# Kernel optimization log

Hardware: AMD Instinct MI355X
Metric: run time of the kernel (lower is better)

Reference implementation:

```python
import jax, jax.numpy as jnp
import numpy as np

H, D, BS = 32, 128, 64          # num_heads, head_dim, gate block_size
GATE_DIM = 64
GATE_TEMP = 2.0                 # _GATE_TARGET_TEMPERATURE
CLAMP_MIN, CLAMP_MAX = -50.0, 50.0


def _rotate_half(x):
    x1, x2 = jnp.split(x, 2, axis=-1)
    return jnp.concatenate([-x2, x1], axis=-1)


def setup_inputs() -> dict:
    key = jax.random.key(0)
    ks = jax.random.split(key, 8)
    B, S, E = 1, 2048, 4096
    hidden_states = jax.random.normal(ks[0], (B, S, E), jnp.float32) * 0.02
    # standard RoPE tables, [B, S, D]
    inv_freq = 1.0 / (10000.0 ** (jnp.arange(0, D, 2, dtype=jnp.float32) / D))
    freqs = jnp.arange(S, dtype=jnp.float32)[:, None] * inv_freq[None, :]
    emb = jnp.concatenate([freqs, freqs], axis=-1)
    cos = jnp.broadcast_to(jnp.cos(emb)[None], (B, S, D)).astype(jnp.float32)
    sin = jnp.broadcast_to(jnp.sin(emb)[None], (B, S, D)).astype(jnp.float32)
    Wq = jax.random.normal(ks[1], (E, E), jnp.float32) * 0.02
    Wk = jax.random.normal(ks[2], (E, E), jnp.float32) * 0.02
    Wv = jax.random.normal(ks[3], (E, E), jnp.float32) * 0.02
    Wo = jax.random.normal(ks[4], (E, E), jnp.float32) * 0.02
    Wg_q = jax.random.normal(ks[5], (GATE_DIM, D), jnp.float32) * 0.05
    Wg_k = jax.random.normal(ks[6], (GATE_DIM, D), jnp.float32) * 0.05
    return {"hidden_states": hidden_states, "cos": cos, "sin": sin,
            "Wq": Wq, "Wk": Wk, "Wv": Wv, "Wo": Wo,
            "Wg_q": Wg_q, "Wg_k": Wg_k}


def reference(hidden_states, cos, sin, Wq, Wk, Wv, Wo, Wg_q, Wg_k):
    B, S, E = hidden_states.shape
    scale = np.float32(1.0 / np.sqrt(D))

    # ---- base attention (training path: full dense attention w/ scores) ----
    q = (hidden_states @ Wq.T).reshape(B, S, H, D).transpose(0, 2, 1, 3)  # [B,H,S,D]
    k = (hidden_states @ Wk.T).reshape(B, S, H, D).transpose(0, 2, 1, 3)
    v = (hidden_states @ Wv.T).reshape(B, S, H, D).transpose(0, 2, 1, 3)

    # _apply_rotary_pos_emb: cos/sin are 3D [B,S,D] -> unsqueeze head dim
    c, s = cos[:, None], sin[:, None]
    q = q * c + _rotate_half(q) * s
    k = k * c + _rotate_half(k) * s

    scores = jnp.einsum('bhqd,bhkd->bhqk', q, k) * scale  # [B,H,S,S]
    causal = jnp.tril(jnp.ones((S, S), dtype=bool))
    scores = jnp.where(causal, scores, -jnp.inf)
    attn = jax.nn.softmax(scores, axis=-1)
    ctx = jnp.einsum('bhqk,bhkd->bhqd', attn, v)
    attn_output = ctx.transpose(0, 2, 1, 3).reshape(B, S, E) @ Wo.T

    # ---- _compute_gate_target: blockwise maxpool -> clamp -> tempered softmax ----
    NB = S // BS  # S divisible by BS, so the -inf padding branch is a no-op
    block_max = scores.reshape(B, H, NB, BS, NB, BS).max(axis=(3, 5))  # [B,H,NB,NB]
    finite = jnp.isfinite(block_max)
    block_max = jnp.where(finite, jnp.clip(block_max, CLAMP_MIN, CLAMP_MAX), block_max)
    gate_target = jax.nn.softmax(
        block_max.reshape(B, H, NB * NB) / GATE_TEMP, axis=-1
    ).reshape(B, H, NB, NB)

    # ---- AttnGate prediction: mean-pooled block Q/K -> low-rank block logits ----
    qb = q.reshape(B, H, NB, BS, D).mean(axis=3)  # [B,H,NB,D]
    kb = k.reshape(B, H, NB, BS, D).mean(axis=3)
    gq = jnp.einsum('bhnd,gd->bhng', qb, Wg_q)
    gk = jnp.einsum('bhnd,gd->bhng', kb, Wg_k)
    glogits = jnp.einsum('bhqg,bhkg->bhqk', gq, gk) * np.float32(1.0 / np.sqrt(GATE_DIM))
    bmask = jnp.tril(jnp.ones((NB, NB), dtype=bool))  # block-causal
    glogits = jnp.where(bmask, glogits, -jnp.inf)
    gate_pred = jax.nn.softmax(
        glogits.reshape(B, H, NB * NB), axis=-1
    ).reshape(B, H, NB, NB)

    return attn_output, gate_pred, gate_target
```

## Files before the change

### kernel.cpp

```cpp
#include <hip/hip_runtime.h>
#include <stdint.h>

#define S_LEN 2048
#define EMB   4096
#define NHEAD 32
#define DHEAD 128
#define NBLK  32
#define GDIM  64

typedef float  f32x4  __attribute__((ext_vector_type(4)));
typedef __bf16 bf16x8 __attribute__((ext_vector_type(8)));
typedef unsigned short u16;

__device__ __forceinline__ u16 f2bf(float f) {
  uint32_t u = __float_as_uint(f);
  u += 0x7fffu + ((u >> 16) & 1u);
  return (u16)(u >> 16);
}
__device__ __forceinline__ float bf2f(u16 u) {
  return __uint_as_float(((uint32_t)u) << 16);
}

__device__ __forceinline__ void ld_lds16(const u16* g, u16* l) {
  __builtin_amdgcn_global_load_lds((const __attribute__((address_space(1))) void*)g,
                                   (__attribute__((address_space(3))) void*)l, 16, 0, 0);
}

__global__ void conv_f32_bf16(const float* __restrict__ in, u16* __restrict__ out, int n4) {
  int i = blockIdx.x * 256 + threadIdx.x;
  if (i >= n4) return;
  float4 v = ((const float4*)in)[i];
  ushort4 o;
  o.x = f2bf(v.x); o.y = f2bf(v.y); o.z = f2bf(v.z); o.w = f2bf(v.w);
  ((ushort4*)out)[i] = o;
}

__global__ void conv3_f32_bf16(const float* __restrict__ a, const float* __restrict__ b,
                               const float* __restrict__ c, u16* __restrict__ oa,
                               u16* __restrict__ ob, u16* __restrict__ oc, int n4) {
  int i = blockIdx.x * 256 + threadIdx.x;
  if (i >= n4) return;
  const float* in = (blockIdx.y == 0) ? a : (blockIdx.y == 1) ? b : c;
  u16* out = (blockIdx.y == 0) ? oa : (blockIdx.y == 1) ? ob : oc;
  float4 v = ((const float4*)in)[i];
  ushort4 o;
  o.x = f2bf(v.x); o.y = f2bf(v.y); o.z = f2bf(v.z); o.w = f2bf(v.w);
  ((ushort4*)out)[i] = o;
}

__global__ void __launch_bounds__(512, 2) qkv_gemm_256(
    const u16* __restrict__ A, const u16* __restrict__ Bq, const u16* __restrict__ Bk,
    const u16* __restrict__ Bv, u16* __restrict__ outq, u16* __restrict__ outk,
    u16* __restrict__ outvt, const float* __restrict__ cosp, const float* __restrict__ sinp)
{
  extern __shared__ u16 lds[];

  const int tid  = threadIdx.x;
  const int w    = tid >> 6;
  const int lane = tid & 63;
  const int r    = lane & 15;
  const int qd   = lane >> 4;
  const int wr   = w >> 2;
  const int wc   = w & 3;
  const int hh   = wc >> 1;

  const int which = blockIdx.x >> 4;
  const int nt    = blockIdx.x & 15;
  const int m0    = blockIdx.y * 256;
  const int n0    = nt * 256;
  const int K     = EMB;
  const u16* Bm = (which == 0) ? Bq : (which == 1) ? Bk : Bv;

  const int swz0 = (qd ^ (r & 7)) * 8;
  const int swz1 = ((4 + qd) ^ (r & 7)) * 8;
  const int rowbaseA = (wr * 64 + r) * 64;
  const int rowbaseB = (hh * 64 + (wc & 1) * 16 + r) * 64;

  const int srw = tid >> 3;
  const int sgs = ((tid & 7) ^ (srw & 7)) * 8;
  const u16* pA0 = A + (size_t)(m0 + srw) * K + sgs;
  const int fm = ((srw >> 5) & 1) * 64 + (srw & 31);
  const u16* pB0 = Bm + (size_t)(n0 + fm) * K + sgs;

  f32x4 acc[8][4];
#pragma unroll
  for (int mi = 0; mi < 8; ++mi)
#pragma unroll
    for (int ni = 0; ni < 4; ++ni) acc[mi][ni] = (f32x4){0.f, 0.f, 0.f, 0.f};

  auto stA = [&](int tt, int half) {
    u16* d = lds + ((tt & 1) * 2 + half) * 8192 + w * 512;
    const u16* g = pA0 + (size_t)(half * 128) * K + tt * 64;
    ld_lds16(g, d);
    ld_lds16(g + (size_t)64 * K, d + 4096);
  };
  auto stB = [&](int tt, int half) {
    u16* d = lds + 32768 + ((tt & 1) * 2 + half) * 8192 + w * 512;
    const u16* g = pB0 + (size_t)(half * 32) * K + tt * 64;
    ld_lds16(g, d);
    ld_lds16(g + (size_t)128 * K, d + 4096);
  };

  stA(0, 0); stB(0, 0); stB(0, 1); stA(0, 1);
  asm volatile("s_waitcnt vmcnt(0)" ::: "memory");
  __builtin_amdgcn_s_barrier();

  for (int t = 0; t < 64; ++t) {
    const u16* bufA = lds + (t & 1) * 16384;
    const u16* bufB = lds + 32768 + (t & 1) * 16384;
    bf16x8 aF[4][2], bLo[2][2], bHi[2][2];

    {
      const u16* ab = bufA + rowbaseA;
      const u16* bb = bufB + rowbaseB;
#pragma unroll
      for (int mi = 0; mi < 4; ++mi) {
        aF[mi][0] = *(const bf16x8*)(ab + mi * 1024 + swz0);
        aF[mi][1] = *(const bf16x8*)(ab + mi * 1024 + swz1);
      }
#pragma unroll
      for (int ni = 0; ni < 2; ++ni) {
        bLo[ni][0] = *(const bf16x8*)(bb + ni * 2048 + swz0);
        bLo[ni][1] = *(const bf16x8*)(bb + ni * 2048 + swz1);
      }
    }
    if (t < 63) stA(t + 1, 0);
    __builtin_amdgcn_s_barrier();
    asm volatile("s_waitcnt lgkmcnt(0)" ::: "memory");
    __builtin_amdgcn_sched_barrier(0);
    __builtin_amdgcn_s_setprio(1);
#pragma unroll
    for (int mi = 0; mi < 4; ++mi)
#pragma unroll
      for (int ni = 0; ni < 2; ++ni) {
        acc[mi][ni] = __builtin_amdgcn_mfma_f32_16x16x32_bf16(aF[mi][0], bLo[ni][0], acc[mi][ni], 0, 0, 0);
        acc[mi][ni] = __builtin_amdgcn_mfma_f32_16x16x32_bf16(aF[mi][1], bLo[ni][1], acc[mi][ni], 0, 0, 0);
      }
    __builtin_amdgcn_s_setprio(0);
    if (t < 63) asm volatile("s_waitcnt vmcnt(4)" ::: "memory");
    else        asm volatile("s_waitcnt vmcnt(2)" ::: "memory");
    __builtin_amdgcn_s_barrier();

    {
      const u16* bb = bufB + 8192 + rowbaseB;
#pragma unroll
      for (int ni = 0; ni < 2; ++ni) {
        bHi[ni][0] = *(const bf16x8*)(bb + ni * 2048 + swz0);
        bHi[ni][1] = *(const bf16x8*)(bb + ni * 2048 + swz1);
      }
    }
    if (t < 63) stB(t + 1, 0);
    __builtin_amdgcn_s_barrier();
    asm volatile("s_waitcnt lgkmcnt(0)" ::: "memory");
    __builtin_amdgcn_sched_barrier(0);
    __builtin_amdgcn_s_setprio(1);
#pragma unroll
    for (int mi = 0; mi < 4; ++mi)
#pragma unroll
      for (int ni = 0; ni < 2; ++ni) {
        acc[mi][ni + 2] = __builtin_amdgcn_mfma_f32_16x16x32_bf16(aF[mi][0], bHi[ni][0], acc[mi][ni + 2], 0, 0, 0);
        acc[mi][ni + 2] = __builtin_amdgcn_mfma_f32_16x16x32_bf16(aF[mi][1], bHi[ni][1], acc[mi][ni + 2], 0, 0, 0);
      }
    __builtin_amdgcn_s_setprio(0);
    if (t < 63) asm volatile("s_waitcnt vmcnt(4)" ::: "memory");
    else        asm volatile("s_waitcnt vmcnt(0)" ::: "memory");
    __builtin_amdgcn_s_barrier();

    {
      const u16* ab = bufA + 8192 + rowbaseA;
#pragma unroll
      for (int mi = 0; mi < 4; ++mi) {
        aF[mi][0] = *(const bf16x8*)(ab + mi * 1024 + swz0);
        aF[mi][1] = *(const bf16x8*)(ab + mi * 1024 + swz1);
      }
    }
    if (t < 63) stB(t + 1, 1);
    __builtin_amdgcn_s_barrier();
    asm volatile("s_waitcnt lgkmcnt(0)" ::: "memory");
    __builtin_amdgcn_sched_barrier(0);
    __builtin_amdgcn_s_setprio(1);
#pragma unroll
    for (int mi = 0; mi < 4; ++mi)
#pragma unroll
      for (int ni = 0; ni < 2; ++ni) {
        acc[mi + 4][ni + 2] = __builtin_amdgcn_mfma_f32_16x16x32_bf16(aF[mi][0], bHi[ni][0], acc[mi + 4][ni + 2], 0, 0, 0);
        acc[mi + 4][ni + 2] = __builtin_amdgcn_mfma_f32_16x16x32_bf16(aF[mi][1], bHi[ni][1], acc[mi + 4][ni + 2], 0, 0, 0);
      }
    __builtin_amdgcn_s_setprio(0);
    __builtin_amdgcn_s_barrier();

    if (t < 63) stA(t + 1, 1);
    __builtin_amdgcn_s_barrier();
    __builtin_amdgcn_s_setprio(1);
#pragma unroll
    for (int mi = 0; mi < 4; ++mi)
#pragma unroll
      for (int ni = 0; ni < 2; ++ni) {
        acc[mi + 4][ni] = __builtin_amdgcn_mfma_f32_16x16x32_bf16(aF[mi][0], bLo[ni][0], acc[mi + 4][ni], 0, 0, 0);
        acc[mi + 4][ni] = __builtin_amdgcn_mfma_f32_16x16x32_bf16(aF[mi][1], bLo[ni][1], acc[mi + 4][ni], 0, 0, 0);
      }
    __builtin_amdgcn_s_setprio(0);
    if (t < 63) asm volatile("s_waitcnt vmcnt(4)" ::: "memory");
    __builtin_amdgcn_s_barrier();
  }

  if (which < 2) {
    u16* out = which ? outk : outq;
    const int hh_out = 2 * nt + hh;
#pragma unroll
    for (int mi = 0; mi < 8; ++mi) {
      const int rbase = m0 + (mi >> 2) * 128 + wr * 64 + (mi & 3) * 16 + qd * 4;
#pragma unroll
      for (int pp = 0; pp < 2; ++pp) {
        const int dlo = pp * 32 + (wc & 1) * 16 + r;
#pragma unroll
        for (int rg = 0; rg < 4; ++rg) {
          int srow = rbase + rg;
          float c = cosp[srow * DHEAD + dlo];
          float s = sinp[srow * DHEAD + dlo];
          float lo = acc[mi][pp * 2 + 0][rg], hi = acc[mi][pp * 2 + 1][rg];
          size_t base = ((size_t)hh_out * S_LEN + srow) * DHEAD;
          out[base + dlo]      = f2bf(lo * c - hi * s);
          out[base + dlo + 64] = f2bf(hi * c + lo * s);
        }
      }
    }
  } else {
    u16* lT = lds;
#pragma unroll
    for (int ch = 0; ch < 2; ++ch) {
      __syncthreads();
#pragma unroll
      for (int mq = 0; mq < 4; ++mq) {
        const int mi = ch * 4 + mq;
        const int lr = wr * 64 + mq * 16 + qd * 4;
#pragma unroll
        for (int ni = 0; ni < 4; ++ni) {
          const int col = hh * 128 + (ni >> 1) * 32 + (wc & 1) * 16 + (ni & 1) * 64 + r;
#pragma unroll
          for (int rg = 0; rg < 4; ++rg)
            lT[col * 136 + lr + rg] = f2bf(acc[mi][ni][rg]);
        }
      }
      __syncthreads();
      const int c = tid >> 1, sh = (tid & 1) * 64;
      const int hh2 = 2 * nt + (c >> 7), d = c & 127;
      size_t obase = ((size_t)hh2 * DHEAD + d) * S_LEN + m0 + ch * 128 + sh;
#pragma unroll
      for (int i8 = 0; i8 < 8; ++i8) {
        uint4 v = *(const uint4*)&lT[c * 136 + sh + i8 * 8];
        *(uint4*)&outvt[obase + i8 * 8] = v;
      }
    }
  }
}

__global__ void __launch_bounds__(256, 2) gemm_out(
    const u16* __restrict__ A, const u16* __restrict__ B, float* __restrict__ out)
{
  __shared__ u16 lA[128 * 32];
  __shared__ u16 lB[128 * 32];
  const int tid = threadIdx.x;
  const int w = tid >> 6, lane = tid & 63;
  const int r = lane & 15, qd = lane >> 4;
  const int m0 = blockIdx.y * 128, n0 = blockIdx.x * 128;
  const int K = EMB;

  f32x4 acc[2][8];
#pragma unroll
  for (int mi = 0; mi < 2; ++mi)
#pragma unroll
    for (int ni = 0; ni < 8; ++ni) acc[mi][ni] = (f32x4){0.f, 0.f, 0.f, 0.f};

  const u16* Ab = A + (size_t)(m0 + w * 16 + (lane >> 2)) * K + (lane & 3) * 8;
  const u16* Bb = B + (size_t)(n0 + w * 16 + (lane >> 2)) * K + (lane & 3) * 8;
  u16* lAb = &lA[(w * 16) * 32];
  u16* lBb = &lB[(w * 16) * 32];

  for (int k0 = 0; k0 < K; k0 += 32) {
    __syncthreads();
    ld_lds16(Ab + k0, lAb);
    ld_lds16(Ab + (size_t)64 * K + k0, lAb + 64 * 32);
    ld_lds16(Bb + k0, lBb);
    ld_lds16(Bb + (size_t)64 * K + k0, lBb + 64 * 32);
    __syncthreads();
    bf16x8 af0 = *(const bf16x8*)&lA[(w * 32 + r) * 32 + qd * 8];
    bf16x8 af1 = *(const bf16x8*)&lA[(w * 32 + 16 + r) * 32 + qd * 8];
#pragma unroll
    for (int ni = 0; ni < 8; ++ni) {
      bf16x8 bf = *(const bf16x8*)&lB[(ni * 16 + r) * 32 + qd * 8];
      acc[0][ni] = __builtin_amdgcn_mfma_f32_16x16x32_bf16(af0, bf, acc[0][ni], 0, 0, 0);
      acc[1][ni] = __builtin_amdgcn_mfma_f32_16x16x32_bf16(af1, bf, acc[1][ni], 0, 0, 0);
    }
  }
#pragma unroll
  for (int mi = 0; mi < 2; ++mi)
#pragma unroll
    for (int ni = 0; ni < 8; ++ni)
#pragma unroll
      for (int rg = 0; rg < 4; ++rg) {
        int srow = m0 + w * 32 + mi * 16 + qd * 4 + rg;
        out[(size_t)srow * EMB + n0 + ni * 16 + r] = acc[mi][ni][rg];
      }
}

__global__ void __launch_bounds__(256, 2) attn_fwd(
    const u16* __restrict__ qg, const u16* __restrict__ kg, const u16* __restrict__ vtg,
    u16* __restrict__ ctx, float* __restrict__ bmax)
{
  __shared__ u16 lK[2][64 * 128];
  __shared__ u16 lV[2][128 * 64];
  __shared__ u16 lP[64 * 76];
  __shared__ float lBM[4 * NBLK];

  const int tid = threadIdx.x;
  const int w = tid >> 6, lane = tid & 63;
  const int r = lane & 15, qd = lane >> 4;
  const int h = blockIdx.y;
  const u16* ksrc = kg + (size_t)h * S_LEN * DHEAD;
  const u16* vsrc = vtg + (size_t)h * DHEAD * S_LEN;
  const float scale = 0.08838834764831845f;

  const int ksl   = (lane & 15) ^ (w * 4 + (lane >> 4));
  const int krow0 = w * 4 + (lane >> 4);
  const u16* kg0  = ksrc + (size_t)krow0 * DHEAD + ksl * 8;
  const int vsl   = (lane & 7) ^ (lane >> 3);
  const int vrow0 = w * 8 + (lane >> 3);
  const u16* vg0  = vsrc + (size_t)vrow0 * S_LEN + vsl * 8;

  for (int qsel = 0; qsel < 2; ++qsel) {
    const int qb = qsel ? (31 - (int)blockIdx.x) : (int)blockIdx.x;

    auto stage = [&](int kb, int buf) {
      u16* kd = &lK[buf][w * 512];
      const u16* kgp = kg0 + (size_t)kb * 64 * DHEAD;
#pragma unroll
      for (int i = 0; i < 4; ++i) ld_lds16(kgp + i * 16 * DHEAD, kd + i * 2048);
      u16* vd = &lV[buf][w * 512];
      const u16* vgp = vg0 + kb * 64;
#pragma unroll
      for (int i = 0; i < 4; ++i) ld_lds16(vgp + (size_t)i * 32 * S_LEN, vd + i * 2048);
    };

    stage(0, 0);
    bf16x8 qf[4];
    {
      const u16* qp = qg + ((size_t)h * S_LEN + qb * 64 + w * 16 + r) * DHEAD + qd * 8;
#pragma unroll
      for (int ki = 0; ki < 4; ++ki) qf[ki] = *(const bf16x8*)(qp + ki * 32);
    }
    if (qb > 0) stage(1, 1);

    f32x4 o[8];
#pragma unroll
    for (int dt = 0; dt < 8; ++dt) o[dt] = (f32x4){0.f, 0.f, 0.f, 0.f};
    float m_run[4], l_run[4];
#pragma unroll
    for (int rg = 0; rg < 4; ++rg) { m_run[rg] = -__builtin_inff(); l_run[rg] = 0.f; }

    for (int kb = 0; kb <= qb; ++kb) {
      const int buf = kb & 1;
      if (kb < qb) asm volatile("s_waitcnt vmcnt(8)" ::: "memory");
      else         asm volatile("s_waitcnt vmcnt(0)" ::: "memory");
      __builtin_amdgcn_s_barrier();

      f32x4 sf[4];
#pragma unroll
      for (int nt = 0; nt < 4; ++nt) sf[nt] = (f32x4){0.f, 0.f, 0.f, 0.f};
      __builtin_amdgcn_s_setprio(1);
#pragma unroll
      for (int ki = 0; ki < 4; ++ki)
#pragma unroll
        for (int nt = 0; nt < 4; ++nt) {
          bf16x8 bf = *(const bf16x8*)&lK[buf][(nt * 16 + r) * 128 + (((ki << 2) + qd) ^ r) * 8];
          sf[nt] = __builtin_amdgcn_mfma_f32_16x16x32_bf16(qf[ki], bf, sf[nt], 0, 0, 0);
        }
      __builtin_amdgcn_s_setprio(0);

      float rmax[4];
#pragma unroll
      for (int rg = 0; rg < 4; ++rg) rmax[rg] = -__builtin_inff();
#pragma unroll
      for (int nt = 0; nt < 4; ++nt)
#pragma unroll
        for (int rg = 0; rg < 4; ++rg) {
          float s = sf[nt][rg] * scale;
          if (kb == qb) {
            int col = nt * 16 + r, row = w * 16 + qd * 4 + rg;
            if (col > row) s = -__builtin_inff();
          }
          sf[nt][rg] = s;
          rmax[rg] = fmaxf(rmax[rg], s);
        }
#pragma unroll
      for (int rg = 0; rg < 4; ++rg) {
        float v = rmax[rg];
        v = fmaxf(v, __shfl_xor(v, 1));
        v = fmaxf(v, __shfl_xor(v, 2));
        v = fmaxf(v, __shfl_xor(v, 4));
        v = fmaxf(v, __shfl_xor(v, 8));
        rmax[rg] = v;
      }
      {
        float v = fmaxf(fmaxf(rmax[0], rmax[1]), fmaxf(rmax[2], rmax[3]));
        v = fmaxf(v, __shfl_xor(v, 16));
        v = fmaxf(v, __shfl_xor(v, 32));
        if (lane == 0) lBM[w * NBLK + kb] = v;
      }

      float alpha[4], rsum[4];
#pragma unroll
      for (int rg = 0; rg < 4; ++rg) {
        float mn = fmaxf(m_run[rg], rmax[rg]);
        alpha[rg] = __expf(m_run[rg] - mn);
        m_run[rg] = mn;
        rsum[rg] = 0.f;
      }
#pragma unroll
      for (int nt = 0; nt < 4; ++nt)
#pragma unroll
        for (int rg = 0; rg < 4; ++rg) {
          float p = __expf(sf[nt][rg] - m_run[rg]);
          sf[nt][rg] = p;
          rsum[rg] += p;
        }
#pragma unroll
      for (int rg = 0; rg < 4; ++rg) {
        float v = rsum[rg];
        v += __shfl_xor(v, 1);
        v += __shfl_xor(v, 2);
        v += __shfl_xor(v, 4);
        v += __shfl_xor(v, 8);
        l_run[rg] = l_run[rg] * alpha[rg] + v;
      }
#pragma unroll
      for (int nt = 0; nt < 4; ++nt)
#pragma unroll
        for (int rg = 0; rg < 4; ++rg)
          lP[(w * 16 + qd * 4 + rg) * 76 + nt * 16 + r] = f2bf(sf[nt][rg]);
#pragma unroll
      for (int dt = 0; dt < 8; ++dt)
#pragma unroll
        for (int rg = 0; rg < 4; ++rg) o[dt][rg] *= alpha[rg];
      bf16x8 pa0 = *(const bf16x8*)&lP[(w * 16 + r) * 76 + qd * 8];
      bf16x8 pa1 = *(const bf16x8*)&lP[(w * 16 + r) * 76 + 32 + qd * 8];
      __builtin_amdgcn_s_setprio(1);
#pragma unroll
      for (int dt = 0; dt < 8; ++dt) {
        bf16x8 bv0 = *(const bf16x8*)&lV[buf][(dt * 16 + r) * 64 + (qd ^ (r & 7)) * 8];
        bf16x8 bv1 = *(const bf16x8*)&lV[buf][(dt * 16 + r) * 64 + (((4 + qd)) ^ (r & 7)) * 8];
        o[dt] = __builtin_amdgcn_mfma_f32_16x16x32_bf16(pa0, bv0, o[dt], 0, 0, 0);
        o[dt] = __builtin_amdgcn_mfma_f32_16x16x32_bf16(pa1, bv1, o[dt], 0, 0, 0);
      }
      __builtin_amdgcn_s_setprio(0);

      __builtin_amdgcn_s_barrier();
      if (kb + 2 <= qb) stage(kb + 2, buf);
    }

    float inv[4];
#pragma unroll
    for (int rg = 0; rg < 4; ++rg) inv[rg] = 1.f / l_run[rg];
#pragma unroll
    for (int dt = 0; dt < 8; ++dt)
#pragma unroll
      for (int rg = 0; rg < 4; ++rg) {
        int srow = qb * 64 + w * 16 + qd * 4 + rg;
        ctx[(size_t)srow * EMB + h * DHEAD + dt * 16 + r] = f2bf(o[dt][rg] * inv[rg]);
      }
    __syncthreads();
    if (tid <= qb) {
      float v = fmaxf(fmaxf(lBM[0 * NBLK + tid], lBM[1 * NBLK + tid]),
                      fmaxf(lBM[2 * NBLK + tid], lBM[3 * NBLK + tid]));
      bmax[((size_t)h * NBLK + qb) * NBLK + tid] = v;
    }
    __syncthreads();
  }
}

__global__ void bmean2(const u16* __restrict__ q, const u16* __restrict__ k,
                       float* __restrict__ qo, float* __restrict__ ko) {
  int nb = blockIdx.x, h = blockIdx.y, t = threadIdx.x;
  const u16* x = blockIdx.z ? k : q;
  float* out = blockIdx.z ? ko : qo;
  const u16* p = x + ((size_t)h * S_LEN + nb * 64) * DHEAD + t * 2;
  float s0 = 0.f, s1 = 0.f;
#pragma unroll 8
  for (int i = 0; i < 64; ++i) {
    uint32_t v = *(const uint32_t*)(p + (size_t)i * DHEAD);
    s0 += bf2f((u16)v);
    s1 += bf2f((u16)(v >> 16));
  }
  float2 rr = {s0 * (1.f / 64.f), s1 * (1.f / 64.f)};
  *(float2*)&out[((size_t)h * NBLK + nb) * DHEAD + t * 2] = rr;
}

__global__ void __launch_bounds__(256) gate_kernel(
    const float* __restrict__ qm, const float* __restrict__ km,
    const float* __restrict__ Wgq, const float* __restrict__ Wgk,
    const float* __restrict__ bmx, float* __restrict__ gpred, float* __restrict__ gtgt)
{
  __shared__ float gq[NBLK * GDIM], gk[NBLK * GDIM];
  __shared__ float red[256];
  const int h = blockIdx.x, tid = threadIdx.x;

  for (int i = 0; i < 8; ++i) {
    int e = tid + 256 * i;
    int n = e >> 6, g = e & 63;
    const float* qrow = qm + ((size_t)h * NBLK + n) * DHEAD;
    const float* krow = km + ((size_t)h * NBLK + n) * DHEAD;
    const float* wq = Wgq + g * DHEAD;
    const float* wk = Wgk + g * DHEAD;
    float s1 = 0.f, s2 = 0.f;
    for (int d = 0; d < DHEAD; ++d) { s1 += qrow[d] * wq[d]; s2 += krow[d] * wk[d]; }
    gq[e] = s1; gk[e] = s2;
  }
  __syncthreads();

  float gl[4];
  for (int i = 0; i < 4; ++i) {
    int idx = tid + 256 * i;
    int qn = idx >> 5, kn = idx & 31;
    if (kn <= qn) {
      float s = 0.f;
      for (int g = 0; g < GDIM; ++g) s += gq[qn * GDIM + g] * gk[kn * GDIM + g];
      gl[i] = s * 0.125f;
    } else gl[i] = -__builtin_inff();
  }
  float mx = fmaxf(fmaxf(gl[0], gl[1]), fmaxf(gl[2], gl[3]));
  red[tid] = mx; __syncthreads();
  for (int st = 128; st > 0; st >>= 1) { if (tid < st) red[tid] = fmaxf(red[tid], red[tid + st]); __syncthreads(); }
  float gmax = red[0]; __syncthreads();
  float ex[4], lsum = 0.f;
  for (int i = 0; i < 4; ++i) { ex[i] = __expf(gl[i] - gmax); lsum += ex[i]; }
  red[tid] = lsum; __syncthreads();
  for (int st = 128; st > 0; st >>= 1) { if (tid < st) red[tid] += red[tid + st]; __syncthreads(); }
  float invs = 1.f / red[0]; __syncthreads();
  for (int i = 0; i < 4; ++i) gpred[(size_t)h * 1024 + tid + 256 * i] = ex[i] * invs;

  float tl[4];
  for (int i = 0; i < 4; ++i) {
    int idx = tid + 256 * i;
    int qn = idx >> 5, kn = idx & 31;
    tl[i] = (kn <= qn) ? fminf(fmaxf(bmx[(size_t)h * 1024 + idx], -50.f), 50.f) * 0.5f
                       : -__builtin_inff();
  }
  float mx2 = fmaxf(fmaxf(tl[0], tl[1]), fmaxf(tl[2], tl[3]));
  red[tid] = mx2; __syncthreads();
  for (int st = 128; st > 0; st >>= 1) { if (tid < st) red[tid] = fmaxf(red[tid], red[tid + st]); __syncthreads(); }
  float tmax = red[0]; __syncthreads();
  float ex2[4], ls2 = 0.f;
  for (int i = 0; i < 4; ++i) { ex2[i] = __expf(tl[i] - tmax); ls2 += ex2[i]; }
  red[tid] = ls2; __syncthreads();
  for (int st = 128; st > 0; st >>= 1) { if (tid < st) red[tid] += red[tid + st]; __syncthreads(); }
  float inv2 = 1.f / red[0];
  for (int i = 0; i < 4; ++i) gtgt[(size_t)h * 1024 + tid + 256 * i] = ex2[i] * inv2;
}

extern "C" void kernel_launch(void* const* d_in, const int* in_sizes, int n_in,
                              void* d_out, int out_size, void* d_ws, size_t ws_size,
                              hipStream_t stream) {
  const float* hidden = (const float*)d_in[0];
  const float* cosp   = (const float*)d_in[1];
  const float* sinp   = (const float*)d_in[2];
  const float* Wq     = (const float*)d_in[3];
  const float* Wk     = (const float*)d_in[4];
  const float* Wv     = (const float*)d_in[5];
  const float* Wo     = (const float*)d_in[6];
  const float* Wgq    = (const float*)d_in[7];
  const float* Wgk    = (const float*)d_in[8];

  char* ws = (char*)d_ws;
  u16* wqb = (u16*)ws;
  u16* wkb = (u16*)(ws + 33554432);
  u16* hid = (u16*)(ws + 67108864);
  u16* qbf = (u16*)(ws + 83886080);
  u16* kbf = (u16*)(ws + 100663296);
  u16* vtb = (u16*)(ws + 117440512);
  float* bmx = (float*)(ws + 33554432);
  float* qmn = (float*)(ws + 33554432 + 131072);
  float* kmn = (float*)(ws + 33554432 + 655360);
  u16* ctx = hid;
  u16* wvb = (u16*)d_out;

  float* attn_out = (float*)d_out;
  float* gpred = attn_out + (size_t)S_LEN * EMB;
  float* gtgt  = gpred + NHEAD * NBLK * NBLK;

  conv3_f32_bf16<<<dim3(16384, 3), 256, 0, stream>>>(Wq, Wk, Wv, wqb, wkb, wvb, 4194304);
  conv_f32_bf16<<<8192, 256, 0, stream>>>(hidden, hid, 2097152);

  static bool attr_set = false;
  if (!attr_set) {
    (void)hipFuncSetAttribute((const void*)qkv_gemm_256,
                              hipFuncAttributeMaxDynamicSharedMemorySize, 131072);
    attr_set = true;
  }
  qkv_gemm_256<<<dim3(48, 8), 512, 131072, stream>>>(hid, wqb, wkb, wvb, qbf, kbf, vtb, cosp, sinp);

  conv_f32_bf16<<<16384, 256, 0, stream>>>(Wo, wqb, 4194304);

  attn_fwd<<<dim3(16, NHEAD), 256, 0, stream>>>(qbf, kbf, vtb, ctx, bmx);

  bmean2<<<dim3(NBLK, NHEAD, 2), 128, 0, stream>>>(qbf, kbf, qmn, kmn);
  gate_kernel<<<NHEAD, 256, 0, stream>>>(qmn, kmn, Wgq, Wgk, bmx, gpred, gtgt);

  gemm_out<<<dim3(32, 16), 256, 0, stream>>>(ctx, wqb, attn_out);
}
```

Measured before the change: 762.7 us.

## Shrink QKV GEMM tile to 256x128 with simpler single-stage prefetch loop

The fused QKV projection GEMM moves from 256x256 to 256x128 output tiles, doubling the grid to 768 blocks. The interleaved four-phase LDS/MFMA schedule is replaced by one stage per K step: issue the next tile's global-to-LDS loads, read fragments, run all MFMAs, then wait and barrier. Each block now covers one head, so the RoPE and V-transpose epilogues are simpler and LDS use drops to 96KB. The cost is lower arithmetic intensity per tile and less overlap of memory waits with compute, in exchange for more parallel blocks and fewer barriers.

```diff
diff --git a/kernel.cpp b/kernel.cpp
--- a/kernel.cpp
+++ b/kernel.cpp
@@ -60,166 +60,106 @@
   const int lane = tid & 63;
   const int r    = lane & 15;
   const int qd   = lane >> 4;
-  const int wr   = w >> 2;
-  const int wc   = w & 3;
-  const int hh   = wc >> 1;
-
-  const int which = blockIdx.x >> 4;
-  const int nt    = blockIdx.x & 15;
+  const int wr   = w >> 1;
+  const int wn   = w & 1;
+
+  const int which = blockIdx.x >> 5;
+  const int nt    = blockIdx.x & 31;
   const int m0    = blockIdx.y * 256;
-  const int n0    = nt * 256;
+  const int n0    = nt * 128;
   const int K     = EMB;
   const u16* Bm = (which == 0) ? Bq : (which == 1) ? Bk : Bv;
 
   const int swz0 = (qd ^ (r & 7)) * 8;
   const int swz1 = ((4 + qd) ^ (r & 7)) * 8;
   const int rowbaseA = (wr * 64 + r) * 64;
-  const int rowbaseB = (hh * 64 + (wc & 1) * 16 + r) * 64;
+  const int rowbaseB = (wn * 32 + r) * 64;
 
   const int srw = tid >> 3;
   const int sgs = ((tid & 7) ^ (srw & 7)) * 8;
   const u16* pA0 = A + (size_t)(m0 + srw) * K + sgs;
-  const int fm = ((srw >> 5) & 1) * 64 + (srw & 31);
-  const u16* pB0 = Bm + (size_t)(n0 + fm) * K + sgs;
-
-  f32x4 acc[8][4];
-#pragma unroll
-  for (int mi = 0; mi < 8; ++mi)
+  const u16* pB0 = Bm + (size_t)(n0 + srw) * K + sgs;
+
+  f32x4 acc[4][4];
+#pragma unroll
+  for (int mi = 0; mi < 4; ++mi)
 #pragma unroll
     for (int ni = 0; ni < 4; ++ni) acc[mi][ni] = (f32x4){0.f, 0.f, 0.f, 0.f};
 
-  auto stA = [&](int tt, int half) {
-    u16* d = lds + ((tt & 1) * 2 + half) * 8192 + w * 512;
-    const u16* g = pA0 + (size_t)(half * 128) * K + tt * 64;
+  auto stA = [&](int tt) {
+    u16* d = lds + (tt & 1) * 16384 + w * 512;
+    const u16* g = pA0 + tt * 64;
+    ld_lds16(g, d);
+    ld_lds16(g + (size_t)64 * K, d + 4096);
+    ld_lds16(g + (size_t)128 * K, d + 8192);
+    ld_lds16(g + (size_t)192 * K, d + 12288);
+  };
+  auto stB = [&](int tt) {
+    u16* d = lds + 32768 + (tt & 1) * 8192 + w * 512;
+    const u16* g = pB0 + tt * 64;
     ld_lds16(g, d);
     ld_lds16(g + (size_t)64 * K, d + 4096);
   };
-  auto stB = [&](int tt, int half) {
-    u16* d = lds + 32768 + ((tt & 1) * 2 + half) * 8192 + w * 512;
-    const u16* g = pB0 + (size_t)(half * 32) * K + tt * 64;
-    ld_lds16(g, d);
-    ld_lds16(g + (size_t)128 * K, d + 4096);
-  };
-
-  stA(0, 0); stB(0, 0); stB(0, 1); stA(0, 1);
+
+  stA(0); stB(0);
   asm volatile("s_waitcnt vmcnt(0)" ::: "memory");
   __builtin_amdgcn_s_barrier();
 
   for (int t = 0; t < 64; ++t) {
     const u16* bufA = lds + (t & 1) * 16384;
-    const u16* bufB = lds + 32768 + (t & 1) * 16384;
-    bf16x8 aF[4][2], bLo[2][2], bHi[2][2];
-
+    const u16* bufB = lds + 32768 + (t & 1) * 8192;
+    if (t < 63) { stA(t + 1); stB(t + 1); }
+
+    bf16x8 aF[4][2], bF[4][2];
     {
       const u16* ab = bufA + rowbaseA;
-      const u16* bb = bufB + rowbaseB;
 #pragma unroll
       for (int mi = 0; mi < 4; ++mi) {
         aF[mi][0] = *(const bf16x8*)(ab + mi * 1024 + swz0);
         aF[mi][1] = *(const bf16x8*)(ab + mi * 1024 + swz1);
       }
-#pragma unroll
-      for (int ni = 0; ni < 2; ++ni) {
-        bLo[ni][0] = *(const bf16x8*)(bb + ni * 2048 + swz0);
-        bLo[ni][1] = *(const bf16x8*)(bb + ni * 2048 + swz1);
-      }
-    }
-    if (t < 63) stA(t + 1, 0);
-    __builtin_amdgcn_s_barrier();
-    asm volatile("s_waitcnt lgkmcnt(0)" ::: "memory");
-    __builtin_amdgcn_sched_barrier(0);
+      const u16* bb = bufB + rowbaseB;
+      bF[0][0] = *(const bf16x8*)(bb + swz0);
+      bF[0][1] = *(const bf16x8*)(bb + swz1);
+      bF[1][0] = *(const bf16x8*)(bb + 1024 + swz0);
+      bF[1][1] = *(const bf16x8*)(bb + 1024 + swz1);
+      bF[2][0] = *(const bf16x8*)(bb + 4096 + swz0);
+      bF[2][1] = *(const bf16x8*)(bb + 4096 + swz1);
+      bF[3][0] = *(const bf16x8*)(bb + 5120 + swz0);
+      bF[3][1] = *(const bf16x8*)(bb + 5120 + swz1);
+    }
+
     __builtin_amdgcn_s_setprio(1);
 #pragma unroll
     for (int mi = 0; mi < 4; ++mi)
 #pragma unroll
-      for (int ni = 0; ni < 2; ++ni) {
-        acc[mi][ni] = __builtin_amdgcn_mfma_f32_16x16x32_bf16(aF[mi][0], bLo[ni][0], acc[mi][ni], 0, 0, 0);
-        acc[mi][ni] = __builtin_amdgcn_mfma_f32_16x16x32_bf16(aF[mi][1], bLo[ni][1], acc[mi][ni], 0, 0, 0);
+      for (int ni = 0; ni < 4; ++ni) {
+        acc[mi][ni] = __builtin_amdgcn_mfma_f32_16x16x32_bf16(aF[mi][0], bF[ni][0], acc[mi][ni], 0, 0, 0);
+        acc[mi][ni] = __builtin_amdgcn_mfma_f32_16x16x32_bf16(aF[mi][1], bF[ni][1], acc[mi][ni], 0, 0, 0);
       }
     __builtin_amdgcn_s_setprio(0);
-    if (t < 63) asm volatile("s_waitcnt vmcnt(4)" ::: "memory");
-    else        asm volatile("s_waitcnt vmcnt(2)" ::: "memory");
-    __builtin_amdgcn_s_barrier();
-
-    {
-      const u16* bb = bufB + 8192 + rowbaseB;
-#pragma unroll
-      for (int ni = 0; ni < 2; ++ni) {
-        bHi[ni][0] = *(const bf16x8*)(bb + ni * 2048 + swz0);
-        bHi[ni][1] = *(const bf16x8*)(bb + ni * 2048 + swz1);
-      }
-    }
-    if (t < 63) stB(t + 1, 0);
-    __builtin_amdgcn_s_barrier();
-    asm volatile("s_waitcnt lgkmcnt(0)" ::: "memory");
-    __builtin_amdgcn_sched_barrier(0);
-    __builtin_amdgcn_s_setprio(1);
-#pragma unroll
-    for (int mi = 0; mi < 4; ++mi)
-#pragma unroll
-      for (int ni = 0; ni < 2; ++ni) {
-        acc[mi][ni + 2] = __builtin_amdgcn_mfma_f32_16x16x32_bf16(aF[mi][0], bHi[ni][0], acc[mi][ni + 2], 0, 0, 0);
-        acc[mi][ni + 2] = __builtin_amdgcn_mfma_f32_16x16x32_bf16(aF[mi][1], bHi[ni][1], acc[mi][ni + 2], 0, 0, 0);
-      }
-    __builtin_amdgcn_s_setprio(0);
-    if (t < 63) asm volatile("s_waitcnt vmcnt(4)" ::: "memory");
-    else        asm volatile("s_waitcnt vmcnt(0)" ::: "memory");
-    __builtin_amdgcn_s_barrier();
-
-    {
-      const u16* ab = bufA + 8192 + rowbaseA;
-#pragma unroll
-      for (int mi = 0; mi < 4; ++mi) {
-        aF[mi][0] = *(const bf16x8*)(ab + mi * 1024 + swz0);
-        aF[mi][1] = *(const bf16x8*)(ab + mi * 1024 + swz1);
-      }
-    }
-    if (t < 63) stB(t + 1, 1);
-    __builtin_amdgcn_s_barrier();
-    asm volatile("s_waitcnt lgkmcnt(0)" ::: "memory");
-    __builtin_amdgcn_sched_barrier(0);
-    __builtin_amdgcn_s_setprio(1);
-#pragma unroll
-    for (int mi = 0; mi < 4; ++mi)
-#pragma unroll
-      for (int ni = 0; ni < 2; ++ni) {
-        acc[mi + 4][ni + 2] = __builtin_amdgcn_mfma_f32_16x16x32_bf16(aF[mi][0], bHi[ni][0], acc[mi + 4][ni + 2], 0, 0, 0);
-        acc[mi + 4][ni + 2] = __builtin_amdgcn_mfma_f32_16x16x32_bf16(aF[mi][1], bHi[ni][1], acc[mi + 4][ni + 2], 0, 0, 0);
-      }
-    __builtin_amdgcn_s_setprio(0);
-    __builtin_amdgcn_s_barrier();
-
-    if (t < 63) stA(t + 1, 1);
-    __builtin_amdgcn_s_barrier();
-    __builtin_amdgcn_s_setprio(1);
-#pragma unroll
-    for (int mi = 0; mi < 4; ++mi)
-#pragma unroll
-      for (int ni = 0; ni < 2; ++ni) {
-        acc[mi + 4][ni] = __builtin_amdgcn_mfma_f32_16x16x32_bf16(aF[mi][0], bLo[ni][0], acc[mi + 4][ni], 0, 0, 0);
-        acc[mi + 4][ni] = __builtin_amdgcn_mfma_f32_16x16x32_bf16(aF[mi][1], bLo[ni][1], acc[mi + 4][ni], 0, 0, 0);
-      }
-    __builtin_amdgcn_s_setprio(0);
-    if (t < 63) asm volatile("s_waitcnt vmcnt(4)" ::: "memory");
-    __builtin_amdgcn_s_barrier();
+
+    if (t < 63) {
+      asm volatile("s_waitcnt vmcnt(0)" ::: "memory");
+      __builtin_amdgcn_s_barrier();
+    }
   }
 
   if (which < 2) {
     u16* out = which ? outk : outq;
-    const int hh_out = 2 * nt + hh;
-#pragma unroll
-    for (int mi = 0; mi < 8; ++mi) {
-      const int rbase = m0 + (mi >> 2) * 128 + wr * 64 + (mi & 3) * 16 + qd * 4;
+#pragma unroll
+    for (int mi = 0; mi < 4; ++mi) {
+      const int rbase = m0 + wr * 64 + mi * 16 + qd * 4;
 #pragma unroll
       for (int pp = 0; pp < 2; ++pp) {
-        const int dlo = pp * 32 + (wc & 1) * 16 + r;
+        const int dlo = wn * 32 + pp * 16 + r;
 #pragma unroll
         for (int rg = 0; rg < 4; ++rg) {
           int srow = rbase + rg;
           float c = cosp[srow * DHEAD + dlo];
           float s = sinp[srow * DHEAD + dlo];
-          float lo = acc[mi][pp * 2 + 0][rg], hi = acc[mi][pp * 2 + 1][rg];
-          size_t base = ((size_t)hh_out * S_LEN + srow) * DHEAD;
+          float lo = acc[mi][pp][rg], hi = acc[mi][pp + 2][rg];
+          size_t base = ((size_t)nt * S_LEN + srow) * DHEAD;
           out[base + dlo]      = f2bf(lo * c - hi * s);
           out[base + dlo + 64] = f2bf(hi * c + lo * s);
         }
@@ -227,30 +167,25 @@
     }
   } else {
     u16* lT = lds;
-#pragma unroll
-    for (int ch = 0; ch < 2; ++ch) {
-      __syncthreads();
-#pragma unroll
-      for (int mq = 0; mq < 4; ++mq) {
-        const int mi = ch * 4 + mq;
-        const int lr = wr * 64 + mq * 16 + qd * 4;
-#pragma unroll
-        for (int ni = 0; ni < 4; ++ni) {
-          const int col = hh * 128 + (ni >> 1) * 32 + (wc & 1) * 16 + (ni & 1) * 64 + r;
-#pragma unroll
-          for (int rg = 0; rg < 4; ++rg)
-            lT[col * 136 + lr + rg] = f2bf(acc[mi][ni][rg]);
-        }
-      }
-      __syncthreads();
-      const int c = tid >> 1, sh = (tid & 1) * 64;
-      const int hh2 = 2 * nt + (c >> 7), d = c & 127;
-      size_t obase = ((size_t)hh2 * DHEAD + d) * S_LEN + m0 + ch * 128 + sh;
-#pragma unroll
-      for (int i8 = 0; i8 < 8; ++i8) {
-        uint4 v = *(const uint4*)&lT[c * 136 + sh + i8 * 8];
-        *(uint4*)&outvt[obase + i8 * 8] = v;
-      }
+    __syncthreads();
+#pragma unroll
+    for (int mi = 0; mi < 4; ++mi) {
+      const int lrow = wr * 64 + mi * 16 + qd * 4;
+#pragma unroll
+      for (int ni = 0; ni < 4; ++ni) {
+        const int col = wn * 32 + (ni & 1) * 16 + (ni >> 1) * 64 + r;
+#pragma unroll
+        for (int rg = 0; rg < 4; ++rg)
+          lT[col * 264 + lrow + rg] = f2bf(acc[mi][ni][rg]);
+      }
+    }
+    __syncthreads();
+#pragma unroll
+    for (int i8 = 0; i8 < 8; ++i8) {
+      const int flat = tid + i8 * 512;
+      const int d = flat >> 5, sb = flat & 31;
+      uint4 v = *(const uint4*)&lT[d * 264 + sb * 8];
+      *(uint4*)&outvt[((size_t)nt * DHEAD + d) * S_LEN + m0 + sb * 8] = v;
     }
   }
 }
@@ -593,10 +528,10 @@
   static bool attr_set = false;
   if (!attr_set) {
     (void)hipFuncSetAttribute((const void*)qkv_gemm_256,
-                              hipFuncAttributeMaxDynamicSharedMemorySize, 131072);
+                              hipFuncAttributeMaxDynamicSharedMemorySize, 98304);
     attr_set = true;
   }
-  qkv_gemm_256<<<dim3(48, 8), 512, 131072, stream>>>(hid, wqb, wkb, wvb, qbf, kbf, vtb, cosp, sinp);
+  qkv_gemm_256<<<dim3(96, 8), 512, 98304, stream>>>(hid, wqb, wkb, wvb, qbf, kbf, vtb, cosp, sinp);
 
   conv_f32_bf16<<<16384, 256, 0, stream>>>(Wo, wqb, 4194304);
 
```

Result: no change. 753.2 us (-1.2%).
